# Kernel optimization log

Hardware: AMD Instinct MI355X
Metric: run time of the kernel (lower is better)

Reference implementation:

```python
import jax, jax.numpy as jnp
import numpy as np

LATENT, CTX, HID, TDIM, HEADS = 512, 512, 1024, 128, 8
HEAD_DIM = HID // HEADS
SCALE = HEAD_DIM ** -0.5


def _ln(x, g, b, eps=1e-5):
    m = jnp.mean(x, axis=-1, keepdims=True)
    v = jnp.mean((x - m) ** 2, axis=-1, keepdims=True)
    return (x - m) * jax.lax.rsqrt(v + eps) * g + b


def _time_embed(t):
    half = TDIM // 2
    exponent = jnp.linspace(0.0, 1.0, half, dtype=t.dtype)
    freqs = jnp.exp(jnp.log(1000.0) * exponent)
    ang = 2.0 * jnp.pi * t[:, None] * freqs[None, :]
    return jnp.concatenate([jnp.sin(ang), jnp.cos(ang)], axis=-1)  # [B, TDIM]


def setup_inputs() -> dict:
    key = jax.random.key(0)
    ks = iter(jax.random.split(key, 32))
    B, M = 4096, 64

    def w(k, i, o):
        return jax.random.normal(k, (i, o), jnp.float32) * 0.02

    inp = {
        "states": jax.random.normal(next(ks), (B, LATENT), jnp.float32),
        "time_values": jax.random.uniform(next(ks), (B,), jnp.float32),
        "class_summary": jax.random.normal(next(ks), (B, CTX), jnp.float32),
        "support_memory": jax.random.normal(next(ks), (B, M, LATENT), jnp.float32),
        # state_trunk: LN(latent+tdim) -> Linear -> GELU -> Linear
        "trunk_ln_g": jnp.ones((LATENT + TDIM,)), "trunk_ln_b": jnp.zeros((LATENT + TDIM,)),
        "trunk_w1": w(next(ks), LATENT + TDIM, HID), "trunk_b1": jnp.zeros((HID,)),
        "trunk_w2": w(next(ks), HID, HID), "trunk_b2": jnp.zeros((HID,)),
        # memory adapter: LN(latent) -> Linear(latent, hid)
        "mem_ln_g": jnp.ones((LATENT,)), "mem_ln_b": jnp.zeros((LATENT,)),
        "mem_w": w(next(ks), LATENT, HID), "mem_b": jnp.zeros((HID,)),
        # attention projections
        "wq": w(next(ks), HID, HID), "bq": jnp.zeros((HID,)),
        "wk": w(next(ks), HID, HID), "bk": jnp.zeros((HID,)),
        "wv": w(next(ks), HID, HID), "bv": jnp.zeros((HID,)),
        "wo": w(next(ks), HID, HID), "bo": jnp.zeros((HID,)),
        # pre-condition norm + FiLM
        "pre_ln_g": jnp.ones((HID,)), "pre_ln_b": jnp.zeros((HID,)),
        "film_w": w(next(ks), CTX, 2 * HID), "film_b": jnp.zeros((2 * HID,)),
        # conditioner: LN -> Linear -> GELU -> Linear
        "cond_ln_g": jnp.ones((HID,)), "cond_ln_b": jnp.zeros((HID,)),
        "cond_w1": w(next(ks), HID, HID), "cond_b1": jnp.zeros((HID,)),
        "cond_w2": w(next(ks), HID, HID), "cond_b2": jnp.zeros((HID,)),
        # output head: LN -> Linear -> GELU -> Linear(hid, latent)
        "head_ln_g": jnp.ones((HID,)), "head_ln_b": jnp.zeros((HID,)),
        "head_w1": w(next(ks), HID, HID), "head_b1": jnp.zeros((HID,)),
        "head_w2": w(next(ks), HID, LATENT), "head_b2": jnp.zeros((LATENT,)),
    }
    return inp


def _forward(states, time_values, class_summary, support_memory,
             trunk_ln_g, trunk_ln_b, trunk_w1, trunk_b1, trunk_w2, trunk_b2,
             mem_ln_g, mem_ln_b, mem_w, mem_b,
             wq, bq, wk, bk, wv, bv, wo, bo,
             pre_ln_g, pre_ln_b, film_w, film_b,
             cond_ln_g, cond_ln_b, cond_w1, cond_b1, cond_w2, cond_b2,
             head_ln_g, head_ln_b, head_w1, head_b1, head_w2, head_b2):
    B, M, _ = support_memory.shape
    gelu = lambda x: jax.nn.gelu(x, approximate=False)

    # trunk: g = Trunk([y, gamma(t)])
    te = _time_embed(time_values)
    x = _ln(jnp.concatenate([states, te], axis=-1), trunk_ln_g, trunk_ln_b)
    g = gelu(x @ trunk_w1 + trunk_b1) @ trunk_w2 + trunk_b2  # [B, HID]

    # encode memory + single-query multi-head attention
    mem_h = _ln(support_memory, mem_ln_g, mem_ln_b) @ mem_w + mem_b  # [B, M, HID]
    q = (g @ wq + bq).reshape(B, HEADS, HEAD_DIM)
    k = (mem_h @ wk + bk).reshape(B, M, HEADS, HEAD_DIM)
    v = (mem_h @ wv + bv).reshape(B, M, HEADS, HEAD_DIM)
    logits = jnp.einsum("bhd,bmhd->bhm", q, k) * SCALE
    attn = jax.nn.softmax(logits, axis=-1)
    summary = jnp.einsum("bhm,bmhd->bhd", attn, v).reshape(B, HID)
    attn_summary = summary @ wo + bo

    # FiLM conditioning
    combined = _ln(g + attn_summary, pre_ln_g, pre_ln_b)
    film = class_summary @ film_w + film_b
    scale, shift = film[:, :HID], film[:, HID:]
    combined = (1.0 + scale) * combined + shift
    cond_x = _ln(combined, cond_ln_g, cond_ln_b)
    conditioned = gelu(cond_x @ cond_w1 + cond_b1) @ cond_w2 + cond_b2 + combined

    # output head
    hx = _ln(conditioned, head_ln_g, head_ln_b)
    return gelu(hx @ head_w1 + head_b1) @ head_w2 + head_b2  # [B, LATENT]


def reference(states, time_values, class_summary, support_memory,
              trunk_ln_g, trunk_ln_b, trunk_w1, trunk_b1, trunk_w2, trunk_b2,
              mem_ln_g, mem_ln_b, mem_w, mem_b,
              wq, bq, wk, bk, wv, bv, wo, bo,
              pre_ln_g, pre_ln_b, film_w, film_b,
              cond_ln_g, cond_ln_b, cond_w1, cond_b1, cond_w2, cond_b2,
              head_ln_g, head_ln_b, head_w1, head_b1, head_w2, head_b2):
    return _forward(states, time_values, class_summary, support_memory,
                    trunk_ln_g, trunk_ln_b, trunk_w1, trunk_b1, trunk_w2, trunk_b2,
                    mem_ln_g, mem_ln_b, mem_w, mem_b,
                    wq, bq, wk, bk, wv, bv, wo, bo,
                    pre_ln_g, pre_ln_b, film_w, film_b,
                    cond_ln_g, cond_ln_b, cond_w1, cond_b1, cond_w2, cond_b2,
                    head_ln_g, head_ln_b, head_w1, head_b1, head_w2, head_b2)
```

## Files before the change

kernel.cpp:

```cpp
#include <hip/hip_runtime.h>
#include <cstdint>
#include <cstddef>

typedef unsigned short ushort_t;
typedef short s16x8 __attribute__((ext_vector_type(8)));
typedef float f32x4 __attribute__((ext_vector_type(4)));

__device__ __forceinline__ float bf2f(ushort_t h){
  union { unsigned int u; float f; } v; v.u = ((unsigned int)h) << 16; return v.f;
}
__device__ __forceinline__ ushort_t f2bf(float x){
  union { float f; unsigned int u; } v; v.f = x;
  unsigned int r = v.u + 0x7FFFu + ((v.u >> 16) & 1u);
  return (ushort_t)(r >> 16);
}
__device__ __forceinline__ float gelu_f(float x){
  return 0.5f * x * (1.0f + erff(x * 0.7071067811865475f));
}
__device__ __forceinline__ float wave_sum(float v){
  #pragma unroll
  for (int o = 32; o; o >>= 1) v += __shfl_xor(v, o);
  return v;
}
__device__ __forceinline__ void block_reduce2(float& s, float& q, float* red){
  s = wave_sum(s); q = wave_sum(q);
  int w = threadIdx.x >> 6, lane = threadIdx.x & 63, nw = blockDim.x >> 6;
  if (lane == 0){ red[w] = s; red[8 + w] = q; }
  __syncthreads();
  float ts = 0.f, tq = 0.f;
  for (int i = 0; i < nw; ++i){ ts += red[i]; tq += red[8 + i]; }
  __syncthreads();
  s = ts; q = tq;
}

#define SSLOT(cc, m) (((cc) & 56) | (((cc) & 7) ^ (((m) ^ ((m) >> 3)) & 7)))

struct TDesc { const float* in; ushort_t* out; int K; int N; int start; };
struct PrepArgs {
  const float* states; const float* tv; const float* lng; const float* lnb; ushort_t* xnb;
  TDesc t[11];
  int ntiles_end;
  int cast1_blocks;
  int cast_end;
  const float* memw; ushort_t* memwb;
  const float* csum; ushort_t* csb;
  const float* memb; const float* wv; const float* bvp; float* bv2;
};

__global__ __launch_bounds__(256) void prep_k(PrepArgs a){
  int bid = blockIdx.x, tid = threadIdx.x;
  __shared__ float buf[640];
  __shared__ float red[16];
  __shared__ float tbuf[32][33];
  if (bid < 4096){
    int row = bid;
    float t = a.tv[row];
    for (int i = tid; i < 640; i += 256){
      float v;
      if (i < 512) v = a.states[(size_t)row * 512 + i];
      else {
        int j = i - 512, jj = j & 63;
        float fr = expf(6.907755278982137f * ((float)jj * (1.0f / 63.0f)));
        float ang = 6.283185307179586f * t * fr;
        v = (j < 64) ? sinf(ang) : cosf(ang);
      }
      buf[i] = v;
    }
    __syncthreads();
    float s = 0.f, q = 0.f;
    for (int i = tid; i < 640; i += 256){ float v = buf[i]; s += v; q += v * v; }
    block_reduce2(s, q, red);
    float mean = s * (1.0f / 640.0f);
    float var = q * (1.0f / 640.0f) - mean * mean;
    float rstd = rsqrtf(var + 1e-5f);
    for (int i = tid; i < 640; i += 256)
      a.xnb[(size_t)row * 640 + i] = f2bf((buf[i] - mean) * rstd * a.lng[i] + a.lnb[i]);
    return;
  }
  bid -= 4096;
  if (bid < a.ntiles_end){
    int d = 0;
    #pragma unroll
    for (int i = 1; i < 11; ++i) if (bid >= a.t[i].start) d = i;
    TDesc td = a.t[d];
    int tile = bid - td.start;
    int tilesx = td.N >> 5;
    int n0 = (tile % tilesx) << 5, k0 = (tile / tilesx) << 5;
    int tx = tid & 31, ty = tid >> 5;
    #pragma unroll
    for (int j = 0; j < 32; j += 8)
      tbuf[ty + j][tx] = td.in[(size_t)(k0 + ty + j) * td.N + (n0 + tx)];
    __syncthreads();
    #pragma unroll
    for (int j = 0; j < 32; j += 8)
      td.out[(size_t)(n0 + ty + j) * td.K + (k0 + tx)] = f2bf(tbuf[tx][ty + j]);
  } else if (bid < a.cast_end){
    int ci = bid - a.ntiles_end;
    const float* src; ushort_t* dst; int i;
    if (ci < a.cast1_blocks){ src = a.memw; dst = a.memwb; i = ci * 1024 + tid * 4; }
    else { src = a.csum; dst = a.csb; i = (ci - a.cast1_blocks) * 1024 + tid * 4; }
    float4 v = *(const float4*)(src + i);
    union { ushort_t u[4]; uint2 p; } pk;
    pk.u[0] = f2bf(v.x); pk.u[1] = f2bf(v.y); pk.u[2] = f2bf(v.z); pk.u[3] = f2bf(v.w);
    *(uint2*)(dst + i) = pk.p;
  } else {
    int col = (bid - a.cast_end) * 256 + tid;
    float a0 = 0.f, a1 = 0.f, a2 = 0.f, a3 = 0.f;
    for (int j = 0; j < 1024; j += 4){
      a0 += a.memb[j + 0] * a.wv[(size_t)(j + 0) * 1024 + col];
      a1 += a.memb[j + 1] * a.wv[(size_t)(j + 1) * 1024 + col];
      a2 += a.memb[j + 2] * a.wv[(size_t)(j + 2) * 1024 + col];
      a3 += a.memb[j + 3] * a.wv[(size_t)(j + 3) * 1024 + col];
    }
    a.bv2[col] = a0 + a1 + a2 + a3 + a.bvp[col];
  }
}

__global__ __launch_bounds__(256) void ln_rows_k(const ushort_t* __restrict__ in, const float* __restrict__ g,
    const float* __restrict__ b, ushort_t* __restrict__ out, int D){
  int row = blockIdx.x, tid = threadIdx.x, i = tid * 4;
  __shared__ float red[16];
  union { uint2 p; ushort_t u[4]; } vv;
  vv.p = *(const uint2*)(in + (size_t)row * D + i);
  float v[4] = { bf2f(vv.u[0]), bf2f(vv.u[1]), bf2f(vv.u[2]), bf2f(vv.u[3]) };
  float s = v[0] + v[1] + v[2] + v[3];
  float q = v[0]*v[0] + v[1]*v[1] + v[2]*v[2] + v[3]*v[3];
  block_reduce2(s, q, red);
  float invD = 1.0f / (float)D;
  float mean = s * invD, var = q * invD - mean * mean, rstd = rsqrtf(var + 1e-5f);
  union { ushort_t u[4]; uint2 p; } pk;
  #pragma unroll
  for (int e = 0; e < 4; ++e) pk.u[e] = f2bf((v[e] - mean) * rstd * g[i + e] + b[i + e]);
  *(uint2*)(out + (size_t)row * D + i) = pk.p;
}

__global__ __launch_bounds__(256) void fuse_film_k(const ushort_t* __restrict__ combb, const ushort_t* __restrict__ filmb,
    const float* __restrict__ pg, const float* __restrict__ pb,
    const float* __restrict__ cg, const float* __restrict__ cb,
    ushort_t* __restrict__ c2b, ushort_t* __restrict__ cxb){
  int row = blockIdx.x, tid = threadIdx.x, i = tid * 4;
  __shared__ float red[16];
  union { uint2 p; ushort_t u[4]; } av;
  av.p = *(const uint2*)(combb + (size_t)row * 1024 + i);
  float x[4] = { bf2f(av.u[0]), bf2f(av.u[1]), bf2f(av.u[2]), bf2f(av.u[3]) };
  float s = x[0] + x[1] + x[2] + x[3];
  float q = x[0]*x[0] + x[1]*x[1] + x[2]*x[2] + x[3]*x[3];
  block_reduce2(s, q, red);
  float mean = s * (1.0f / 1024.0f), var = q * (1.0f / 1024.0f) - mean * mean;
  float rstd = rsqrtf(var + 1e-5f);
  float4 pgv = *(const float4*)(pg + i), pbv = *(const float4*)(pb + i);
  union { uint2 p; ushort_t u[4]; } scv, shv;
  scv.p = *(const uint2*)(filmb + (size_t)row * 2048 + i);
  shv.p = *(const uint2*)(filmb + (size_t)row * 2048 + 1024 + i);
  float c2[4];
  {
    float pgx[4] = { pgv.x, pgv.y, pgv.z, pgv.w };
    float pbx[4] = { pbv.x, pbv.y, pbv.z, pbv.w };
    #pragma unroll
    for (int e = 0; e < 4; ++e){
      float cc = (x[e] - mean) * rstd * pgx[e] + pbx[e];
      c2[e] = (1.0f + bf2f(scv.u[e])) * cc + bf2f(shv.u[e]);
    }
  }
  union { ushort_t u[4]; uint2 p; } pc;
  #pragma unroll
  for (int e = 0; e < 4; ++e) pc.u[e] = f2bf(c2[e]);
  *(uint2*)(c2b + (size_t)row * 1024 + i) = pc.p;
  float s2 = c2[0] + c2[1] + c2[2] + c2[3];
  float q2 = c2[0]*c2[0] + c2[1]*c2[1] + c2[2]*c2[2] + c2[3]*c2[3];
  block_reduce2(s2, q2, red);
  float m2 = s2 * (1.0f / 1024.0f), v2 = q2 * (1.0f / 1024.0f) - m2 * m2;
  float r2 = rsqrtf(v2 + 1e-5f);
  float4 cgv = *(const float4*)(cg + i), cbv = *(const float4*)(cb + i);
  union { ushort_t u[4]; uint2 p; } pk;
  pk.u[0] = f2bf((c2[0] - m2) * r2 * cgv.x + cbv.x);
  pk.u[1] = f2bf((c2[1] - m2) * r2 * cgv.y + cbv.y);
  pk.u[2] = f2bf((c2[2] - m2) * r2 * cgv.z + cbv.z);
  pk.u[3] = f2bf((c2[3] - m2) * r2 * cgv.w + cbv.w);
  *(uint2*)(cxb + (size_t)row * 1024 + i) = pk.p;
}

__global__ __launch_bounds__(256, 2) void suppattn_k(
    const float* __restrict__ support, const float* __restrict__ lgw, const float* __restrict__ lbw,
    const ushort_t* __restrict__ U, ushort_t* __restrict__ R)
{
  __shared__ ushort_t S[64 * 512];
  __shared__ ushort_t UG[9 * 512];
  __shared__ float WTf[8][65];
  __shared__ float SUMV[64], SUMSQ[64];
  __shared__ __align__(16) float MEANR[64];
  __shared__ __align__(16) float RSTDR[64];
  __shared__ float PMAX[4][8], PSUM[4][8], PMU[4][8];
  __shared__ float AB[2][8];
  __shared__ float MUH[8];

  int bb = blockIdx.x, tid = threadIdx.x, w = tid >> 6, l = tid & 63;
  const ushort_t* Ub = U + (size_t)bb * 4096;

  for (int id = tid; id < 576; id += 256){
    int hr8 = id >> 6, cc = id & 63;
    int byteoff = hr8 * 1024 + (((cc & 56) | ((cc & 7) ^ (hr8 & 7))) << 4);
    uint4* dst = (uint4*)((char*)UG + byteoff);
    if (hr8 < 8){
      s16x8 uv = *(const s16x8*)(Ub + hr8 * 512 + cc * 8);
      float4 g0 = *(const float4*)(lgw + cc * 8);
      float4 g1 = *(const float4*)(lgw + cc * 8 + 4);
      float ga[8] = { g0.x, g0.y, g0.z, g0.w, g1.x, g1.y, g1.z, g1.w };
      union { ushort_t u[8]; uint4 p; } pk;
      #pragma unroll
      for (int e = 0; e < 8; ++e) pk.u[e] = f2bf(ga[e] * bf2f((ushort_t)uv[e]));
      *dst = pk.p;
    } else {
      *dst = make_uint4(0x3F803F80u, 0x3F803F80u, 0x3F803F80u, 0x3F803F80u);
    }
  }

  {
    int h0 = 2 * w, h1 = 2 * w + 1;
    s16x8 u0 = *(const s16x8*)(Ub + h0 * 512 + l * 8);
    s16x8 u1 = *(const s16x8*)(Ub + h1 * 512 + l * 8);
    float4 g0 = *(const float4*)(lgw + l * 8), g1 = *(const float4*)(lgw + l * 8 + 4);
    float4 c0 = *(const float4*)(lbw + l * 8), c1 = *(const float4*)(lbw + l * 8 + 4);
    float ga[8] = { g0.x, g0.y, g0.z, g0.w, g1.x, g1.y, g1.z, g1.w };
    float ba[8] = { c0.x, c0.y, c0.z, c0.w, c1.x, c1.y, c1.z, c1.w };
    float A0 = 0.f, B0 = 0.f, A1 = 0.f, B1 = 0.f;
    #pragma unroll
    for (int e = 0; e < 8; ++e){
      float x0 = bf2f((ushort_t)u0[e]), x1 = bf2f((ushort_t)u1[e]);
      A0 += ba[e] * x0; B0 += ga[e] * x0;
      A1 += ba[e] * x1; B1 += ga[e] * x1;
    }
    A0 = wave_sum(A0); B0 = wave_sum(B0); A1 = wave_sum(A1); B1 = wave_sum(B1);
    if (l == 0){ AB[0][h0] = A0; AB[1][h0] = B0; AB[0][h1] = A1; AB[1][h1] = B1; }
  }

  #pragma unroll 4
  for (int i = 0; i < 16; ++i){
    int m = i * 4 + w;
    const float* row = support + ((size_t)bb * 64 + m) * 512 + l * 8;
    float4 a0 = *(const float4*)row, a1 = *(const float4*)(row + 4);
    union { ushort_t u[8]; uint4 p; } pk;
    pk.u[0] = f2bf(a0.x); pk.u[1] = f2bf(a0.y); pk.u[2] = f2bf(a0.z); pk.u[3] = f2bf(a0.w);
    pk.u[4] = f2bf(a1.x); pk.u[5] = f2bf(a1.y); pk.u[6] = f2bf(a1.z); pk.u[7] = f2bf(a1.w);
    int byteoff = m * 1024 + (SSLOT(l, m) << 4);
    *(uint4*)((char*)S + byteoff) = pk.p;
  }
  __syncthreads();

  int l15 = l & 15, lk = l >> 4;
  int hr = (l15 < 8) ? l15 : 8;
  int arowb = (w * 16 + l15) * 1024;
  int hrowb = hr * 1024;
  int am = w * 16 + l15;
  f32x4 dacc = (f32x4){0.f, 0.f, 0.f, 0.f};
  f32x4 sacc = (f32x4){0.f, 0.f, 0.f, 0.f};
  #pragma unroll
  for (int ks = 0; ks < 16; ++ks){
    int cc = ks * 4 + lk;
    s16x8 afr = *(const s16x8*)((char*)S + arowb + (SSLOT(cc, am) << 4));
    s16x8 bfr = *(const s16x8*)((char*)UG + hrowb + (((cc & 56) | ((cc & 7) ^ (hr & 7))) << 4));
    dacc = __builtin_amdgcn_mfma_f32_16x16x32_bf16(afr, bfr, dacc, 0, 0, 0);
    sacc = __builtin_amdgcn_mfma_f32_16x16x32_bf16(afr, afr, sacc, 0, 0, 0);
  }
  if (l15 == 8){
    #pragma unroll
    for (int j = 0; j < 4; ++j) SUMV[w * 16 + lk * 4 + j] = dacc[j];
  }
  if ((l15 >> 2) == lk) SUMSQ[w * 16 + l15] = sacc[l15 & 3];
  __syncthreads();
  if (tid < 64){
    float mean = SUMV[tid] * (1.0f / 512.0f);
    float var = SUMSQ[tid] * (1.0f / 512.0f) - mean * mean;
    MEANR[tid] = mean;
    RSTDR[tid] = rsqrtf(var + 1e-5f);
  }
  __syncthreads();

  int r0 = w * 16 + lk * 4;
  float4 mns = *(const float4*)(MEANR + r0);
  float4 rst = *(const float4*)(RSTDR + r0);
  float mn[4] = { mns.x, mns.y, mns.z, mns.w };
  float rs[4] = { rst.x, rst.y, rst.z, rst.w };
  float Ah = AB[0][l15 & 7], Bh = AB[1][l15 & 7];
  float lg[4];
  #pragma unroll
  for (int j = 0; j < 4; ++j)
    lg[j] = 0.08838834764831845f * (rs[j] * (dacc[j] - mn[j] * Bh) + Ah);
  float lmax = fmaxf(fmaxf(lg[0], lg[1]), fmaxf(lg[2], lg[3]));
  lmax = fmaxf(lmax, __shfl_xor(lmax, 16));
  lmax = fmaxf(lmax, __shfl_xor(lmax, 32));
  if (l < 8) PMAX[w][l] = lmax;
  __syncthreads();
  float gmax = fmaxf(fmaxf(PMAX[0][l15 & 7], PMAX[1][l15 & 7]),
                     fmaxf(PMAX[2][l15 & 7], PMAX[3][l15 & 7]));
  float e4[4]; float ls = 0.f, lm = 0.f;
  #pragma unroll
  for (int j = 0; j < 4; ++j){
    e4[j] = __expf(lg[j] - gmax);
    ls += e4[j];
    lm += e4[j] * rs[j] * mn[j];
  }
  ls += __shfl_xor(ls, 16); ls += __shfl_xor(ls, 32);
  lm += __shfl_xor(lm, 16); lm += __shfl_xor(lm, 32);
  if (l < 8){ PSUM[w][l] = ls; PMU[w][l] = lm; }
  __syncthreads();
  float Sh = PSUM[0][l15 & 7] + PSUM[1][l15 & 7] + PSUM[2][l15 & 7] + PSUM[3][l15 & 7];
  float inv = 1.0f / Sh;
  if (l15 < 8){
    #pragma unroll
    for (int j = 0; j < 4; ++j) WTf[l15][r0 + j] = e4[j] * rs[j] * inv;
  }
  if (w == 0 && l < 8){
    MUH[l] = (PMU[0][l] + PMU[1][l] + PMU[2][l] + PMU[3][l]) * inv;
  }
  __syncthreads();

  union { ushort_t u[8]; s16x8 v; } af0, af1;
  af0.v = (s16x8){0,0,0,0,0,0,0,0};
  af1.v = (s16x8){0,0,0,0,0,0,0,0};
  if (l15 < 8){
    #pragma unroll
    for (int e = 0; e < 8; ++e){
      af0.u[e] = f2bf(WTf[l15][lk * 8 + e]);
      af1.u[e] = f2bf(WTf[l15][32 + lk * 8 + e]);
    }
  }
  float mu[4];
  #pragma unroll
  for (int j = 0; j < 4; ++j) mu[j] = (lk < 2) ? MUH[lk * 4 + j] : 0.f;

  const char* Sp = (const char*)S;
  #pragma unroll
  for (int ns = 0; ns < 8; ++ns){
    int c = w * 128 + ns * 16 + l15;
    int cch = c >> 3, cb = (c & 7) * 2;
    int sb = cch & 56, cl = cch & 7;
    union { ushort_t u[8]; s16x8 v; } bf0, bf1;
    #pragma unroll
    for (int e = 0; e < 8; ++e){
      int m0 = lk * 8 + e;
      int m1 = m0 + 32;
      bf0.u[e] = *(const ushort_t*)(Sp + m0 * 1024 + ((sb | (cl ^ ((m0 ^ lk) & 7))) << 4) + cb);
      bf1.u[e] = *(const ushort_t*)(Sp + m1 * 1024 + ((sb | (cl ^ ((m1 ^ (4 + lk)) & 7))) << 4) + cb);
    }
    f32x4 cacc = (f32x4){0.f, 0.f, 0.f, 0.f};
    cacc = __builtin_amdgcn_mfma_f32_16x16x32_bf16(af0.v, bf0.v, cacc, 0, 0, 0);
    cacc = __builtin_amdgcn_mfma_f32_16x16x32_bf16(af1.v, bf1.v, cacc, 0, 0, 0);
    if (lk < 2){
      float gc = lgw[c], bc = lbw[c];
      #pragma unroll
      for (int j = 0; j < 4; ++j){
        int h = lk * 4 + j;
        R[(size_t)bb * 4096 + h * 512 + c] = f2bf(gc * (cacc[j] - mu[j]) + bc);
      }
    }
  }
}

#define GLL16(gsrc, ldst) \
  __builtin_amdgcn_global_load_lds((const __attribute__((address_space(1))) unsigned int*)(gsrc), \
                                   (__attribute__((address_space(3))) unsigned int*)(ldst), 16, 0, 0)

template<bool GELU, bool BIAS, bool WF32, bool WBF16, bool RESID>
__global__ __launch_bounds__(256, 3) void gemm_k(
    const ushort_t* __restrict__ A, int lda, long long aZ,
    const ushort_t* __restrict__ Bt, int ldb, long long bZ,
    const float* __restrict__ bias, long long biasZ,
    float* __restrict__ C, int ldc, long long cZ,
    ushort_t* __restrict__ Cb, int ldcb, long long cbZ,
    const ushort_t* __restrict__ R, int ldr,
    int M, int N, int K)
{
  __shared__ ushort_t smA[2][64 * 64];
  __shared__ ushort_t smB[2][128 * 64];
  int tid = threadIdx.x, lane = tid & 63, w = tid >> 6;
  int z = blockIdx.z;
  A  += (size_t)aZ * z;
  Bt += (size_t)bZ * z;
  if (BIAS)  bias += (size_t)biasZ * z;
  if (WF32)  C    += (size_t)cZ * z;
  if (WBF16) Cb   += (size_t)cbZ * z;

  int gx = gridDim.x, gy = gridDim.y;
  int nwg = gx * gy;
  int bx = blockIdx.x, by = blockIdx.y;
  if ((nwg & 7) == 0 && (gx & (gx - 1)) == 0){
    int lid = bx + gx * by;
    int cpx = nwg >> 3;
    int slid = (lid & 7) * cpx + (lid >> 3);
    int lgx = 31 - __clz(gx);
    bx = slid & (gx - 1);
    by = slid >> lgx;
  }
  int m0 = by * 64, n0 = bx * 128;
  int nk = K >> 6;

  auto stage = [&](int buf, int kt){
    int k0 = kt << 6;
    #pragma unroll
    for (int i = 0; i < 2; ++i){
      int c = ((w << 1) + i) * 64 + lane;
      int rowl = c >> 3, sp = c & 7;
      int sg = sp ^ (rowl & 7);
      GLL16(A + (size_t)(m0 + rowl) * lda + (k0 + sg * 8), &smA[buf][((w << 1) + i) * 512]);
    }
    #pragma unroll
    for (int i = 0; i < 4; ++i){
      int c = ((w << 2) + i) * 64 + lane;
      int rowl = c >> 3, sp = c & 7;
      int sg = sp ^ (rowl & 7);
      GLL16(Bt + (size_t)(n0 + rowl) * ldb + (k0 + sg * 8), &smB[buf][((w << 2) + i) * 512]);
    }
  };

  int qrow = w >> 1, qcol = w & 1;
  int l15 = lane & 15, lk = lane >> 4, l7 = lane & 7;
  int sb0 = ((0 + lk) ^ l7) << 4;
  int sb1 = ((4 + lk) ^ l7) << 4;
  int arow = (qrow * 32 + l15) * 128;
  int brow = (qcol * 64 + l15) * 128;

  f32x4 acc[2][4];
  #pragma unroll
  for (int m = 0; m < 2; ++m)
    #pragma unroll
    for (int n = 0; n < 4; ++n)
      acc[m][n] = (f32x4){0.f, 0.f, 0.f, 0.f};

  stage(0, 0);
  asm volatile("s_waitcnt vmcnt(0)" ::: "memory");
  __syncthreads();
  for (int kt = 0; kt < nk; ++kt){
    int cur = kt & 1;
    if (kt + 1 < nk) stage((kt + 1) & 1, kt + 1);
    const char* ab = (const char*)&smA[cur][0];
    const char* bbp = (const char*)&smB[cur][0];
    s16x8 af[2][2], bfv[4][2];
    #pragma unroll
    for (int m = 0; m < 2; ++m){
      af[m][0] = *(const s16x8*)(ab + arow + m * 2048 + sb0);
      af[m][1] = *(const s16x8*)(ab + arow + m * 2048 + sb1);
    }
    #pragma unroll
    for (int n = 0; n < 4; ++n){
      bfv[n][0] = *(const s16x8*)(bbp + brow + n * 2048 + sb0);
      bfv[n][1] = *(const s16x8*)(bbp + brow + n * 2048 + sb1);
    }
    #pragma unroll
    for (int kb = 0; kb < 2; ++kb)
      #pragma unroll
      for (int m = 0; m < 2; ++m)
        #pragma unroll
        for (int n = 0; n < 4; ++n)
          acc[m][n] = __builtin_amdgcn_mfma_f32_16x16x32_bf16(af[m][kb], bfv[n][kb], acc[m][n], 0, 0, 0);
    asm volatile("s_waitcnt vmcnt(0)" ::: "memory");
    __syncthreads();
  }

  #pragma unroll
  for (int n = 0; n < 4; ++n){
    int col = n0 + qcol * 64 + n * 16 + l15;
    float bvv = BIAS ? bias[col] : 0.0f;
    #pragma unroll
    for (int m = 0; m < 2; ++m){
      int rbase = m0 + qrow * 32 + m * 16 + lk * 4;
      #pragma unroll
      for (int r = 0; r < 4; ++r){
        float x = acc[m][n][r] + bvv;
        if (GELU) x = gelu_f(x);
        int row = rbase + r;
        if (RESID) x += bf2f(R[(size_t)row * ldr + col]);
        if (WF32)  C[(size_t)row * ldc + col] = x;
        if (WBF16) Cb[(size_t)row * ldcb + col] = f2bf(x);
      }
    }
  }
}

extern "C" void kernel_launch(void* const* d_in, const int* in_sizes, int n_in,
                              void* d_out, int out_size, void* d_ws, size_t ws_size,
                              hipStream_t stream)
{
  (void)in_sizes; (void)n_in; (void)out_size;
  const float* states      = (const float*)d_in[0];
  const float* time_values = (const float*)d_in[1];
  const float* class_sum   = (const float*)d_in[2];
  const float* support     = (const float*)d_in[3];
  const float* trunk_ln_g  = (const float*)d_in[4];
  const float* trunk_ln_b  = (const float*)d_in[5];
  const float* trunk_w1    = (const float*)d_in[6];
  const float* trunk_b1    = (const float*)d_in[7];
  const float* trunk_w2    = (const float*)d_in[8];
  const float* trunk_b2    = (const float*)d_in[9];
  const float* mem_ln_g    = (const float*)d_in[10];
  const float* mem_ln_b    = (const float*)d_in[11];
  const float* mem_w       = (const float*)d_in[12];
  const float* mem_b       = (const float*)d_in[13];
  const float* wq          = (const float*)d_in[14];
  const float* bq          = (const float*)d_in[15];
  const float* wk          = (const float*)d_in[16];
  const float* wv          = (const float*)d_in[18];
  const float* bvp         = (const float*)d_in[19];
  const float* wo          = (const float*)d_in[20];
  const float* bo          = (const float*)d_in[21];
  const float* pre_g       = (const float*)d_in[22];
  const float* pre_b       = (const float*)d_in[23];
  const float* film_w      = (const float*)d_in[24];
  const float* film_b      = (const float*)d_in[25];
  const float* cond_g      = (const float*)d_in[26];
  const float* cond_b      = (const float*)d_in[27];
  const float* cond_w1     = (const float*)d_in[28];
  const float* cond_b1     = (const float*)d_in[29];
  const float* cond_w2     = (const float*)d_in[30];
  const float* cond_b2     = (const float*)d_in[31];
  const float* head_g      = (const float*)d_in[32];
  const float* head_bb     = (const float*)d_in[33];
  const float* head_w1     = (const float*)d_in[34];
  const float* head_b1     = (const float*)d_in[35];
  const float* head_w2     = (const float*)d_in[36];
  const float* head_b2     = (const float*)d_in[37];
  float* out = (float*)d_out;

  char* ws = (char*)d_ws;
  size_t off = 0;
  auto alloc = [&](size_t bytes)->char*{
    char* p = ws + off;
    off += (bytes + 255) & ~(size_t)255;
    return p;
  };
  ushort_t* tw1T   = (ushort_t*)alloc((size_t)640 * 1024 * 2);
  ushort_t* tw2T   = (ushort_t*)alloc((size_t)1024 * 1024 * 2);
  ushort_t* wqT    = (ushort_t*)alloc((size_t)1024 * 1024 * 2);
  ushort_t* wkT    = (ushort_t*)alloc((size_t)1024 * 1024 * 2);
  ushort_t* wvT    = (ushort_t*)alloc((size_t)1024 * 1024 * 2);
  ushort_t* woT    = (ushort_t*)alloc((size_t)1024 * 1024 * 2);
  ushort_t* memw_b = (ushort_t*)alloc((size_t)512 * 1024 * 2);
  ushort_t* filmWT = (ushort_t*)alloc((size_t)512 * 2048 * 2);
  ushort_t* cw1T   = (ushort_t*)alloc((size_t)1024 * 1024 * 2);
  ushort_t* cw2T   = (ushort_t*)alloc((size_t)1024 * 1024 * 2);
  ushort_t* hw1T   = (ushort_t*)alloc((size_t)1024 * 1024 * 2);
  ushort_t* hw2T   = (ushort_t*)alloc((size_t)1024 * 512 * 2);
  ushort_t* K2     = (ushort_t*)alloc((size_t)512 * 1024 * 2);
  ushort_t* V2T    = (ushort_t*)alloc((size_t)1024 * 512 * 2);
  float*    bv2    = (float*)   alloc((size_t)1024 * 4);
  ushort_t* xnb    = (ushort_t*)alloc((size_t)4096 * 640 * 2);
  ushort_t* h1     = (ushort_t*)alloc((size_t)4096 * 1024 * 2);
  ushort_t* gb     = (ushort_t*)alloc((size_t)4096 * 1024 * 2);
  ushort_t* qb     = (ushort_t*)alloc((size_t)4096 * 1024 * 2);
  ushort_t* U      = (ushort_t*)alloc((size_t)4096 * 4096 * 2);
  ushort_t* Rb     = (ushort_t*)alloc((size_t)4096 * 4096 * 2);
  ushort_t* sumb   = (ushort_t*)alloc((size_t)4096 * 1024 * 2);
  ushort_t* combb  = (ushort_t*)alloc((size_t)4096 * 1024 * 2);
  ushort_t* csb    = (ushort_t*)alloc((size_t)4096 * 512 * 2);
  ushort_t* filmb  = (ushort_t*)alloc((size_t)4096 * 2048 * 2);
  ushort_t* c2b    = (ushort_t*)alloc((size_t)4096 * 1024 * 2);
  ushort_t* cxb    = (ushort_t*)alloc((size_t)4096 * 1024 * 2);
  ushort_t* c1     = (ushort_t*)alloc((size_t)4096 * 1024 * 2);
  ushort_t* cond2b = (ushort_t*)alloc((size_t)4096 * 1024 * 2);
  ushort_t* hxb    = (ushort_t*)alloc((size_t)4096 * 1024 * 2);
  ushort_t* h3     = (ushort_t*)alloc((size_t)4096 * 1024 * 2);
  if (off > ws_size) return;

  PrepArgs pa;
  pa.states = states; pa.tv = time_values; pa.lng = trunk_ln_g; pa.lnb = trunk_ln_b; pa.xnb = xnb;
  int s = 0;
  auto setT = [&](int i, const float* in, ushort_t* o, int K, int N){
    pa.t[i].in = in; pa.t[i].out = o; pa.t[i].K = K; pa.t[i].N = N; pa.t[i].start = s;
    s += (N >> 5) * (K >> 5);
  };
  setT(0, trunk_w1, tw1T, 640, 1024);
  setT(1, trunk_w2, tw2T, 1024, 1024);
  setT(2, wq, wqT, 1024, 1024);
  setT(3, wk, wkT, 1024, 1024);
  setT(4, wv, wvT, 1024, 1024);
  setT(5, wo, woT, 1024, 1024);
  setT(6, film_w, filmWT, 512, 2048);
  setT(7, cond_w1, cw1T, 1024, 1024);
  setT(8, cond_w2, cw2T, 1024, 1024);
  setT(9, head_w1, hw1T, 1024, 1024);
  setT(10, head_w2, hw2T, 1024, 512);
  pa.ntiles_end = s;
  pa.cast1_blocks = (512 * 1024) / 1024;
  pa.cast_end = s + pa.cast1_blocks + (4096 * 512) / 1024;
  pa.memw = mem_w; pa.memwb = memw_b;
  pa.csum = class_sum; pa.csb = csb;
  pa.memb = mem_b; pa.wv = wv; pa.bvp = bvp; pa.bv2 = bv2;
  prep_k<<<4096 + pa.cast_end + 4, 256, 0, stream>>>(pa);

  gemm_k<false, false, false, true, false><<<dim3(8, 8, 1), 256, 0, stream>>>(
      memw_b, 1024, 0, wkT, 1024, 0, nullptr, 0, nullptr, 0, 0, K2, 1024, 0, nullptr, 0, 512, 1024, 1024);
  gemm_k<false, false, false, true, false><<<dim3(4, 16, 1), 256, 0, stream>>>(
      wvT, 1024, 0, memw_b, 1024, 0, nullptr, 0, nullptr, 0, 0, V2T, 512, 0, nullptr, 0, 1024, 512, 1024);

  gemm_k<true, true, false, true, false><<<dim3(8, 64, 1), 256, 0, stream>>>(
      xnb, 640, 0, tw1T, 640, 0, trunk_b1, 0, nullptr, 0, 0, h1, 1024, 0, nullptr, 0, 4096, 1024, 640);
  gemm_k<false, true, false, true, false><<<dim3(8, 64, 1), 256, 0, stream>>>(
      h1, 1024, 0, tw2T, 1024, 0, trunk_b2, 0, nullptr, 0, 0, gb, 1024, 0, nullptr, 0, 4096, 1024, 1024);
  gemm_k<false, true, false, true, false><<<dim3(8, 64, 1), 256, 0, stream>>>(
      gb, 1024, 0, wqT, 1024, 0, bq, 0, nullptr, 0, 0, qb, 1024, 0, nullptr, 0, 4096, 1024, 1024);
  gemm_k<false, false, false, true, false><<<dim3(4, 64, 8), 256, 0, stream>>>(
      qb, 1024, 128, K2, 1024, 128, nullptr, 0, nullptr, 0, 0, U, 4096, 512, nullptr, 0, 4096, 512, 128);

  suppattn_k<<<4096, 256, 0, stream>>>(support, mem_ln_g, mem_ln_b, U, Rb);

  gemm_k<false, true, false, true, false><<<dim3(1, 64, 8), 256, 0, stream>>>(
      Rb, 4096, 512, V2T, 512, 65536, bv2, 128, nullptr, 0, 0, sumb, 1024, 128, nullptr, 0, 4096, 128, 512);

  gemm_k<false, true, false, true, true><<<dim3(8, 64, 1), 256, 0, stream>>>(
      sumb, 1024, 0, woT, 1024, 0, bo, 0, nullptr, 0, 0, combb, 1024, 0, gb, 1024, 4096, 1024, 1024);
  gemm_k<false, true, false, true, false><<<dim3(16, 64, 1), 256, 0, stream>>>(
      csb, 512, 0, filmWT, 512, 0, film_b, 0, nullptr, 0, 0, filmb, 2048, 0, nullptr, 0, 4096, 2048, 512);

  fuse_film_k<<<4096, 256, 0, stream>>>(combb, filmb, pre_g, pre_b, cond_g, cond_b, c2b, cxb);

  gemm_k<true, true, false, true, false><<<dim3(8, 64, 1), 256, 0, stream>>>(
      cxb, 1024, 0, cw1T, 1024, 0, cond_b1, 0, nullptr, 0, 0, c1, 1024, 0, nullptr, 0, 4096, 1024, 1024);
  gemm_k<false, true, false, true, true><<<dim3(8, 64, 1), 256, 0, stream>>>(
      c1, 1024, 0, cw2T, 1024, 0, cond_b2, 0, nullptr, 0, 0, cond2b, 1024, 0, c2b, 1024, 4096, 1024, 1024);
  ln_rows_k<<<4096, 256, 0, stream>>>(cond2b, head_g, head_bb, hxb, 1024);
  gemm_k<true, true, false, true, false><<<dim3(8, 64, 1), 256, 0, stream>>>(
      hxb, 1024, 0, hw1T, 1024, 0, head_b1, 0, nullptr, 0, 0, h3, 1024, 0, nullptr, 0, 4096, 1024, 1024);
  gemm_k<false, true, true, false, false><<<dim3(4, 64, 1), 256, 0, stream>>>(
      h3, 1024, 0, hw2T, 1024, 0, head_b2, 0, out, 512, 0, nullptr, 0, 0, nullptr, 0, 4096, 512, 1024);
}
```

Measured before the change: 451.8 us.

## Merge GEMM chains into persistent kernels with software grid barriers

```diff
diff --git a/kernel.cpp b/kernel.cpp
--- a/kernel.cpp
+++ b/kernel.cpp
@@ -116,70 +116,6 @@
   }
 }
 
-__global__ __launch_bounds__(256) void ln_rows_k(const ushort_t* __restrict__ in, const float* __restrict__ g,
-    const float* __restrict__ b, ushort_t* __restrict__ out, int D){
-  int row = blockIdx.x, tid = threadIdx.x, i = tid * 4;
-  __shared__ float red[16];
-  union { uint2 p; ushort_t u[4]; } vv;
-  vv.p = *(const uint2*)(in + (size_t)row * D + i);
-  float v[4] = { bf2f(vv.u[0]), bf2f(vv.u[1]), bf2f(vv.u[2]), bf2f(vv.u[3]) };
-  float s = v[0] + v[1] + v[2] + v[3];
-  float q = v[0]*v[0] + v[1]*v[1] + v[2]*v[2] + v[3]*v[3];
-  block_reduce2(s, q, red);
-  float invD = 1.0f / (float)D;
-  float mean = s * invD, var = q * invD - mean * mean, rstd = rsqrtf(var + 1e-5f);
-  union { ushort_t u[4]; uint2 p; } pk;
-  #pragma unroll
-  for (int e = 0; e < 4; ++e) pk.u[e] = f2bf((v[e] - mean) * rstd * g[i + e] + b[i + e]);
-  *(uint2*)(out + (size_t)row * D + i) = pk.p;
-}
-
-__global__ __launch_bounds__(256) void fuse_film_k(const ushort_t* __restrict__ combb, const ushort_t* __restrict__ filmb,
-    const float* __restrict__ pg, const float* __restrict__ pb,
-    const float* __restrict__ cg, const float* __restrict__ cb,
-    ushort_t* __restrict__ c2b, ushort_t* __restrict__ cxb){
-  int row = blockIdx.x, tid = threadIdx.x, i = tid * 4;
-  __shared__ float red[16];
-  union { uint2 p; ushort_t u[4]; } av;
-  av.p = *(const uint2*)(combb + (size_t)row * 1024 + i);
-  float x[4] = { bf2f(av.u[0]), bf2f(av.u[1]), bf2f(av.u[2]), bf2f(av.u[3]) };
-  float s = x[0] + x[1] + x[2] + x[3];
-  float q = x[0]*x[0] + x[1]*x[1] + x[2]*x[2] + x[3]*x[3];
-  block_reduce2(s, q, red);
-  float mean = s * (1.0f / 1024.0f), var = q * (1.0f / 1024.0f) - mean * mean;
-  float rstd = rsqrtf(var + 1e-5f);
-  float4 pgv = *(const float4*)(pg + i), pbv = *(const float4*)(pb + i);
-  union { uint2 p; ushort_t u[4]; } scv, shv;
-  scv.p = *(const uint2*)(filmb + (size_t)row * 2048 + i);
-  shv.p = *(const uint2*)(filmb + (size_t)row * 2048 + 1024 + i);
-  float c2[4];
-  {
-    float pgx[4] = { pgv.x, pgv.y, pgv.z, pgv.w };
-    float pbx[4] = { pbv.x, pbv.y, pbv.z, pbv.w };
-    #pragma unroll
-    for (int e = 0; e < 4; ++e){
-      float cc = (x[e] - mean) * rstd * pgx[e] + pbx[e];
-      c2[e] = (1.0f + bf2f(scv.u[e])) * cc + bf2f(shv.u[e]);
-    }
-  }
-  union { ushort_t u[4]; uint2 p; } pc;
-  #pragma unroll
-  for (int e = 0; e < 4; ++e) pc.u[e] = f2bf(c2[e]);
-  *(uint2*)(c2b + (size_t)row * 1024 + i) = pc.p;
-  float s2 = c2[0] + c2[1] + c2[2] + c2[3];
-  float q2 = c2[0]*c2[0] + c2[1]*c2[1] + c2[2]*c2[2] + c2[3]*c2[3];
-  block_reduce2(s2, q2, red);
-  float m2 = s2 * (1.0f / 1024.0f), v2 = q2 * (1.0f / 1024.0f) - m2 * m2;
-  float r2 = rsqrtf(v2 + 1e-5f);
-  float4 cgv = *(const float4*)(cg + i), cbv = *(const float4*)(cb + i);
-  union { ushort_t u[4]; uint2 p; } pk;
-  pk.u[0] = f2bf((c2[0] - m2) * r2 * cgv.x + cbv.x);
-  pk.u[1] = f2bf((c2[1] - m2) * r2 * cgv.y + cbv.y);
-  pk.u[2] = f2bf((c2[2] - m2) * r2 * cgv.z + cbv.z);
-  pk.u[3] = f2bf((c2[3] - m2) * r2 * cgv.w + cbv.w);
-  *(uint2*)(cxb + (size_t)row * 1024 + i) = pk.p;
-}
-
 __global__ __launch_bounds__(256, 2) void suppattn_k(
     const float* __restrict__ support, const float* __restrict__ lgw, const float* __restrict__ lbw,
     const ushort_t* __restrict__ U, ushort_t* __restrict__ R)
@@ -196,6 +132,18 @@
 
   int bb = blockIdx.x, tid = threadIdx.x, w = tid >> 6, l = tid & 63;
   const ushort_t* Ub = U + (size_t)bb * 4096;
+
+  #pragma unroll 4
+  for (int i = 0; i < 16; ++i){
+    int m = i * 4 + w;
+    const float* row = support + ((size_t)bb * 64 + m) * 512 + l * 8;
+    float4 a0 = *(const float4*)row, a1 = *(const float4*)(row + 4);
+    union { ushort_t u[8]; uint4 p; } pk;
+    pk.u[0] = f2bf(a0.x); pk.u[1] = f2bf(a0.y); pk.u[2] = f2bf(a0.z); pk.u[3] = f2bf(a0.w);
+    pk.u[4] = f2bf(a1.x); pk.u[5] = f2bf(a1.y); pk.u[6] = f2bf(a1.z); pk.u[7] = f2bf(a1.w);
+    int byteoff = m * 1024 + (SSLOT(l, m) << 4);
+    *(uint4*)((char*)S + byteoff) = pk.p;
+  }
 
   for (int id = tid; id < 576; id += 256){
     int hr8 = id >> 6, cc = id & 63;
@@ -233,18 +181,6 @@
     A0 = wave_sum(A0); B0 = wave_sum(B0); A1 = wave_sum(A1); B1 = wave_sum(B1);
     if (l == 0){ AB[0][h0] = A0; AB[1][h0] = B0; AB[0][h1] = A1; AB[1][h1] = B1; }
   }
-
-  #pragma unroll 4
-  for (int i = 0; i < 16; ++i){
-    int m = i * 4 + w;
-    const float* row = support + ((size_t)bb * 64 + m) * 512 + l * 8;
-    float4 a0 = *(const float4*)row, a1 = *(const float4*)(row + 4);
-    union { ushort_t u[8]; uint4 p; } pk;
-    pk.u[0] = f2bf(a0.x); pk.u[1] = f2bf(a0.y); pk.u[2] = f2bf(a0.z); pk.u[3] = f2bf(a0.w);
-    pk.u[4] = f2bf(a1.x); pk.u[5] = f2bf(a1.y); pk.u[6] = f2bf(a1.z); pk.u[7] = f2bf(a1.w);
-    int byteoff = m * 1024 + (SSLOT(l, m) << 4);
-    *(uint4*)((char*)S + byteoff) = pk.p;
-  }
   __syncthreads();
 
   int l15 = l & 15, lk = l >> 4;
@@ -361,39 +297,58 @@
   __builtin_amdgcn_global_load_lds((const __attribute__((address_space(1))) unsigned int*)(gsrc), \
                                    (__attribute__((address_space(3))) unsigned int*)(ldst), 16, 0, 0)
 
-template<bool GELU, bool BIAS, bool WF32, bool WBF16, bool RESID>
-__global__ __launch_bounds__(256, 3) void gemm_k(
-    const ushort_t* __restrict__ A, int lda, long long aZ,
-    const ushort_t* __restrict__ Bt, int ldb, long long bZ,
-    const float* __restrict__ bias, long long biasZ,
-    float* __restrict__ C, int ldc, long long cZ,
-    ushort_t* __restrict__ Cb, int ldcb, long long cbZ,
-    const ushort_t* __restrict__ R, int ldr,
-    int M, int N, int K)
-{
-  __shared__ ushort_t smA[2][64 * 64];
-  __shared__ ushort_t smB[2][128 * 64];
+struct Seg {
+  const ushort_t* A; const ushort_t* Bt; const float* bias;
+  ushort_t* Cb; float* Cf; const ushort_t* R;
+  int lda, ldb, ldc, ldr, gx, K, flags, startTile;
+};
+#define MAXSEG 14
+#define MAXSTG 8
+struct CoopArgs {
+  Seg seg[MAXSEG];
+  int stage_seg_start[MAXSTG + 1];
+  int stage_ntiles[MAXSTG];
+  int stage_type[MAXSTG];
+  int nstages;
+  unsigned* bar;
+  const ushort_t* combb; const ushort_t* filmb;
+  const float *pg, *pb, *cg, *cbp;
+  ushort_t *c2b, *cxb;
+  const ushort_t* ln_in; const float *ln_g, *ln_b; ushort_t* ln_out;
+};
+
+__device__ __forceinline__ void gbar(unsigned* bar, int nb){
+  __syncthreads();
+  if (threadIdx.x == 0){
+    __threadfence();
+    int x = blockIdx.x & 7;
+    int q = nb >> 3;
+    unsigned gen = __hip_atomic_load(&bar[144], __ATOMIC_ACQUIRE, __HIP_MEMORY_SCOPE_AGENT);
+    unsigned v = __hip_atomic_fetch_add(&bar[x * 16], 1u, __ATOMIC_ACQ_REL, __HIP_MEMORY_SCOPE_AGENT);
+    if ((int)v == q - 1){
+      __hip_atomic_store(&bar[x * 16], 0u, __ATOMIC_RELAXED, __HIP_MEMORY_SCOPE_AGENT);
+      unsigned d = __hip_atomic_fetch_add(&bar[128], 1u, __ATOMIC_ACQ_REL, __HIP_MEMORY_SCOPE_AGENT);
+      if (d == 7u){
+        __hip_atomic_store(&bar[128], 0u, __ATOMIC_RELAXED, __HIP_MEMORY_SCOPE_AGENT);
+        __hip_atomic_fetch_add(&bar[144], 1u, __ATOMIC_RELEASE, __HIP_MEMORY_SCOPE_AGENT);
+      } else {
+        while (__hip_atomic_load(&bar[144], __ATOMIC_ACQUIRE, __HIP_MEMORY_SCOPE_AGENT) == gen)
+          __builtin_amdgcn_s_sleep(2);
+      }
+    } else {
+      while (__hip_atomic_load(&bar[144], __ATOMIC_ACQUIRE, __HIP_MEMORY_SCOPE_AGENT) == gen)
+        __builtin_amdgcn_s_sleep(2);
+    }
+    __threadfence();
+  }
+  __syncthreads();
+}
+
+__device__ __forceinline__ void gemm_tile(ushort_t (*smA)[4096], ushort_t (*smB)[4096],
+                                          const Seg& g, int m0, int n0){
+  __syncthreads();
   int tid = threadIdx.x, lane = tid & 63, w = tid >> 6;
-  int z = blockIdx.z;
-  A  += (size_t)aZ * z;
-  Bt += (size_t)bZ * z;
-  if (BIAS)  bias += (size_t)biasZ * z;
-  if (WF32)  C    += (size_t)cZ * z;
-  if (WBF16) Cb   += (size_t)cbZ * z;
-
-  int gx = gridDim.x, gy = gridDim.y;
-  int nwg = gx * gy;
-  int bx = blockIdx.x, by = blockIdx.y;
-  if ((nwg & 7) == 0 && (gx & (gx - 1)) == 0){
-    int lid = bx + gx * by;
-    int cpx = nwg >> 3;
-    int slid = (lid & 7) * cpx + (lid >> 3);
-    int lgx = 31 - __clz(gx);
-    bx = slid & (gx - 1);
-    by = slid >> lgx;
-  }
-  int m0 = by * 64, n0 = bx * 128;
-  int nk = K >> 6;
+  int nk = g.K >> 6;
 
   auto stage = [&](int buf, int kt){
     int k0 = kt << 6;
@@ -402,14 +357,14 @@
       int c = ((w << 1) + i) * 64 + lane;
       int rowl = c >> 3, sp = c & 7;
       int sg = sp ^ (rowl & 7);
-      GLL16(A + (size_t)(m0 + rowl) * lda + (k0 + sg * 8), &smA[buf][((w << 1) + i) * 512]);
-    }
-    #pragma unroll
-    for (int i = 0; i < 4; ++i){
-      int c = ((w << 2) + i) * 64 + lane;
+      GLL16(g.A + (size_t)(m0 + rowl) * g.lda + (k0 + sg * 8), &smA[buf][((w << 1) + i) * 512]);
+    }
+    #pragma unroll
+    for (int i = 0; i < 2; ++i){
+      int c = ((w << 1) + i) * 64 + lane;
       int rowl = c >> 3, sp = c & 7;
       int sg = sp ^ (rowl & 7);
-      GLL16(Bt + (size_t)(n0 + rowl) * ldb + (k0 + sg * 8), &smB[buf][((w << 2) + i) * 512]);
+      GLL16(g.Bt + (size_t)(n0 + rowl) * g.ldb + (k0 + sg * 8), &smB[buf][((w << 1) + i) * 512]);
     }
   };
 
@@ -418,13 +373,13 @@
   int sb0 = ((0 + lk) ^ l7) << 4;
   int sb1 = ((4 + lk) ^ l7) << 4;
   int arow = (qrow * 32 + l15) * 128;
-  int brow = (qcol * 64 + l15) * 128;
-
-  f32x4 acc[2][4];
+  int brow = (qcol * 32 + l15) * 128;
+
+  f32x4 acc[2][2];
   #pragma unroll
   for (int m = 0; m < 2; ++m)
     #pragma unroll
-    for (int n = 0; n < 4; ++n)
+    for (int n = 0; n < 2; ++n)
       acc[m][n] = (f32x4){0.f, 0.f, 0.f, 0.f};
 
   stage(0, 0);
@@ -435,14 +390,14 @@
     if (kt + 1 < nk) stage((kt + 1) & 1, kt + 1);
     const char* ab = (const char*)&smA[cur][0];
     const char* bbp = (const char*)&smB[cur][0];
-    s16x8 af[2][2], bfv[4][2];
+    s16x8 af[2][2], bfv[2][2];
     #pragma unroll
     for (int m = 0; m < 2; ++m){
       af[m][0] = *(const s16x8*)(ab + arow + m * 2048 + sb0);
       af[m][1] = *(const s16x8*)(ab + arow + m * 2048 + sb1);
     }
     #pragma unroll
-    for (int n = 0; n < 4; ++n){
+    for (int n = 0; n < 2; ++n){
       bfv[n][0] = *(const s16x8*)(bbp + brow + n * 2048 + sb0);
       bfv[n][1] = *(const s16x8*)(bbp + brow + n * 2048 + sb1);
     }
@@ -451,29 +406,120 @@
       #pragma unroll
       for (int m = 0; m < 2; ++m)
         #pragma unroll
-        for (int n = 0; n < 4; ++n)
+        for (int n = 0; n < 2; ++n)
           acc[m][n] = __builtin_amdgcn_mfma_f32_16x16x32_bf16(af[m][kb], bfv[n][kb], acc[m][n], 0, 0, 0);
-    asm volatile("s_waitcnt vmcnt(0)" ::: "memory");
-    __syncthreads();
-  }
-
-  #pragma unroll
-  for (int n = 0; n < 4; ++n){
-    int col = n0 + qcol * 64 + n * 16 + l15;
-    float bvv = BIAS ? bias[col] : 0.0f;
+    if (kt + 1 < nk){
+      asm volatile("s_waitcnt vmcnt(0)" ::: "memory");
+      __syncthreads();
+    }
+  }
+
+  bool fG = g.flags & 1, fB = g.flags & 2, fF = g.flags & 4, fR = g.flags & 16;
+  #pragma unroll
+  for (int n = 0; n < 2; ++n){
+    int col = n0 + qcol * 32 + n * 16 + l15;
+    float bvv = fB ? g.bias[col] : 0.0f;
     #pragma unroll
     for (int m = 0; m < 2; ++m){
       int rbase = m0 + qrow * 32 + m * 16 + lk * 4;
       #pragma unroll
       for (int r = 0; r < 4; ++r){
         float x = acc[m][n][r] + bvv;
-        if (GELU) x = gelu_f(x);
+        if (fG) x = gelu_f(x);
         int row = rbase + r;
-        if (RESID) x += bf2f(R[(size_t)row * ldr + col]);
-        if (WF32)  C[(size_t)row * ldc + col] = x;
-        if (WBF16) Cb[(size_t)row * ldcb + col] = f2bf(x);
+        if (fR) x += bf2f(g.R[(size_t)row * g.ldr + col]);
+        if (fF) g.Cf[(size_t)row * g.ldc + col] = x;
+        else    g.Cb[(size_t)row * g.ldc + col] = f2bf(x);
       }
     }
+  }
+}
+
+__device__ void film_row(const CoopArgs& a, int row, float* red){
+  int tid = threadIdx.x, i = tid * 4;
+  union { uint2 p; ushort_t u[4]; } av;
+  av.p = *(const uint2*)(a.combb + (size_t)row * 1024 + i);
+  float x[4] = { bf2f(av.u[0]), bf2f(av.u[1]), bf2f(av.u[2]), bf2f(av.u[3]) };
+  float s = x[0] + x[1] + x[2] + x[3];
+  float q = x[0]*x[0] + x[1]*x[1] + x[2]*x[2] + x[3]*x[3];
+  block_reduce2(s, q, red);
+  float mean = s * (1.0f / 1024.0f), var = q * (1.0f / 1024.0f) - mean * mean;
+  float rstd = rsqrtf(var + 1e-5f);
+  float4 pgv = *(const float4*)(a.pg + i), pbv = *(const float4*)(a.pb + i);
+  union { uint2 p; ushort_t u[4]; } scv, shv;
+  scv.p = *(const uint2*)(a.filmb + (size_t)row * 2048 + i);
+  shv.p = *(const uint2*)(a.filmb + (size_t)row * 2048 + 1024 + i);
+  float c2[4];
+  {
+    float pgx[4] = { pgv.x, pgv.y, pgv.z, pgv.w };
+    float pbx[4] = { pbv.x, pbv.y, pbv.z, pbv.w };
+    #pragma unroll
+    for (int e = 0; e < 4; ++e){
+      float cc = (x[e] - mean) * rstd * pgx[e] + pbx[e];
+      c2[e] = (1.0f + bf2f(scv.u[e])) * cc + bf2f(shv.u[e]);
+    }
+  }
+  union { ushort_t u[4]; uint2 p; } pc;
+  #pragma unroll
+  for (int e = 0; e < 4; ++e) pc.u[e] = f2bf(c2[e]);
+  *(uint2*)(a.c2b + (size_t)row * 1024 + i) = pc.p;
+  float s2 = c2[0] + c2[1] + c2[2] + c2[3];
+  float q2 = c2[0]*c2[0] + c2[1]*c2[1] + c2[2]*c2[2] + c2[3]*c2[3];
+  block_reduce2(s2, q2, red);
+  float m2 = s2 * (1.0f / 1024.0f), v2 = q2 * (1.0f / 1024.0f) - m2 * m2;
+  float r2 = rsqrtf(v2 + 1e-5f);
+  float4 cgv = *(const float4*)(a.cg + i), cbv = *(const float4*)(a.cbp + i);
+  union { ushort_t u[4]; uint2 p; } pk;
+  pk.u[0] = f2bf((c2[0] - m2) * r2 * cgv.x + cbv.x);
+  pk.u[1] = f2bf((c2[1] - m2) * r2 * cgv.y + cbv.y);
+  pk.u[2] = f2bf((c2[2] - m2) * r2 * cgv.z + cbv.z);
+  pk.u[3] = f2bf((c2[3] - m2) * r2 * cgv.w + cbv.w);
+  *(uint2*)(a.cxb + (size_t)row * 1024 + i) = pk.p;
+}
+
+__device__ void ln_row(const CoopArgs& a, int row, float* red){
+  int tid = threadIdx.x, i = tid * 4;
+  union { uint2 p; ushort_t u[4]; } vv;
+  vv.p = *(const uint2*)(a.ln_in + (size_t)row * 1024 + i);
+  float v[4] = { bf2f(vv.u[0]), bf2f(vv.u[1]), bf2f(vv.u[2]), bf2f(vv.u[3]) };
+  float s = v[0] + v[1] + v[2] + v[3];
+  float q = v[0]*v[0] + v[1]*v[1] + v[2]*v[2] + v[3]*v[3];
+  block_reduce2(s, q, red);
+  float mean = s * (1.0f / 1024.0f), var = q * (1.0f / 1024.0f) - mean * mean;
+  float rstd = rsqrtf(var + 1e-5f);
+  union { ushort_t u[4]; uint2 p; } pk;
+  #pragma unroll
+  for (int e = 0; e < 4; ++e) pk.u[e] = f2bf((v[e] - mean) * rstd * a.ln_g[i + e] + a.ln_b[i + e]);
+  *(uint2*)(a.ln_out + (size_t)row * 1024 + i) = pk.p;
+}
+
+__global__ __launch_bounds__(256, 4) void coop_k(CoopArgs a){
+  __shared__ ushort_t smA[2][4096];
+  __shared__ ushort_t smB[2][4096];
+  __shared__ float red[16];
+  int nb = gridDim.x, bid = blockIdx.x;
+  int q = nb >> 3;
+  int slid = (bid & 7) * q + (bid >> 3);
+
+  for (int st = 0; st < a.nstages; ++st){
+    int type = a.stage_type[st];
+    if (type == 0){
+      int s0 = a.stage_seg_start[st], s1 = a.stage_seg_start[st + 1];
+      int nt = a.stage_ntiles[st];
+      for (int t = slid; t < nt; t += nb){
+        int si = s0;
+        while (si + 1 < s1 && t >= a.seg[si + 1].startTile) ++si;
+        Seg g = a.seg[si];
+        int tl = t - g.startTile;
+        int bx = tl % g.gx, by = tl / g.gx;
+        gemm_tile(smA, smB, g, by * 64, bx * 64);
+      }
+    } else if (type == 1){
+      for (int row = bid; row < 4096; row += nb) film_row(a, row, red);
+    } else {
+      for (int row = bid; row < 4096; row += nb) ln_row(a, row, red);
+    }
+    if (st + 1 < a.nstages) gbar(a.bar, nb);
   }
 }
 
@@ -559,7 +605,10 @@
   ushort_t* cond2b = (ushort_t*)alloc((size_t)4096 * 1024 * 2);
   ushort_t* hxb    = (ushort_t*)alloc((size_t)4096 * 1024 * 2);
   ushort_t* h3     = (ushort_t*)alloc((size_t)4096 * 1024 * 2);
+  unsigned* bar    = (unsigned*)alloc(1024);
   if (off > ws_size) return;
+
+  hipMemsetAsync(bar, 0, 1024, stream);
 
   PrepArgs pa;
   pa.states = states; pa.tv = time_values; pa.lng = trunk_ln_g; pa.lnb = trunk_ln_b; pa.xnb = xnb;
@@ -587,39 +636,65 @@
   pa.memb = mem_b; pa.wv = wv; pa.bvp = bvp; pa.bv2 = bv2;
   prep_k<<<4096 + pa.cast_end + 4, 256, 0, stream>>>(pa);
 
-  gemm_k<false, false, false, true, false><<<dim3(8, 8, 1), 256, 0, stream>>>(
-      memw_b, 1024, 0, wkT, 1024, 0, nullptr, 0, nullptr, 0, 0, K2, 1024, 0, nullptr, 0, 512, 1024, 1024);
-  gemm_k<false, false, false, true, false><<<dim3(4, 16, 1), 256, 0, stream>>>(
-      wvT, 1024, 0, memw_b, 1024, 0, nullptr, 0, nullptr, 0, 0, V2T, 512, 0, nullptr, 0, 1024, 512, 1024);
-
-  gemm_k<true, true, false, true, false><<<dim3(8, 64, 1), 256, 0, stream>>>(
-      xnb, 640, 0, tw1T, 640, 0, trunk_b1, 0, nullptr, 0, 0, h1, 1024, 0, nullptr, 0, 4096, 1024, 640);
-  gemm_k<false, true, false, true, false><<<dim3(8, 64, 1), 256, 0, stream>>>(
-      h1, 1024, 0, tw2T, 1024, 0, trunk_b2, 0, nullptr, 0, 0, gb, 1024, 0, nullptr, 0, 4096, 1024, 1024);
-  gemm_k<false, true, false, true, false><<<dim3(8, 64, 1), 256, 0, stream>>>(
-      gb, 1024, 0, wqT, 1024, 0, bq, 0, nullptr, 0, 0, qb, 1024, 0, nullptr, 0, 4096, 1024, 1024);
-  gemm_k<false, false, false, true, false><<<dim3(4, 64, 8), 256, 0, stream>>>(
-      qb, 1024, 128, K2, 1024, 128, nullptr, 0, nullptr, 0, 0, U, 4096, 512, nullptr, 0, 4096, 512, 128);
+  int occ = 0;
+  int nb = 256;
+  if (hipOccupancyMaxActiveBlocksPerMultiprocessor(&occ, coop_k, 256, 0) == hipSuccess && occ >= 1){
+    nb = occ * 256;
+    if (nb > 1024) nb = 1024;
+  }
+  nb &= ~7;
+  if (nb < 8) nb = 8;
+
+  auto mkseg = [](const ushort_t* A, const ushort_t* Bt, const float* bias, ushort_t* Cb, float* Cf,
+                  const ushort_t* R, int lda, int ldb, int ldc, int ldr, int gx, int K, int flags, int start)->Seg{
+    Seg g; g.A = A; g.Bt = Bt; g.bias = bias; g.Cb = Cb; g.Cf = Cf; g.R = R;
+    g.lda = lda; g.ldb = ldb; g.ldc = ldc; g.ldr = ldr; g.gx = gx; g.K = K; g.flags = flags; g.startTile = start;
+    return g;
+  };
+
+  {
+    CoopArgs a{};
+    a.seg[0]  = mkseg(memw_b, wkT, nullptr, K2, nullptr, nullptr, 1024, 1024, 1024, 0, 16, 1024, 0, 0);
+    a.seg[1]  = mkseg(wvT, memw_b, nullptr, V2T, nullptr, nullptr, 1024, 1024, 512, 0, 8, 1024, 0, 128);
+    a.seg[2]  = mkseg(csb, filmWT, film_b, filmb, nullptr, nullptr, 512, 512, 2048, 0, 32, 512, 2, 256);
+    a.seg[3]  = mkseg(xnb, tw1T, trunk_b1, h1, nullptr, nullptr, 640, 640, 1024, 0, 16, 640, 1|2, 2304);
+    a.seg[4]  = mkseg(h1, tw2T, trunk_b2, gb, nullptr, nullptr, 1024, 1024, 1024, 0, 16, 1024, 2, 0);
+    a.seg[5]  = mkseg(gb, wqT, bq, qb, nullptr, nullptr, 1024, 1024, 1024, 0, 16, 1024, 2, 0);
+    for (int z = 0; z < 8; ++z)
+      a.seg[6 + z] = mkseg(qb + z * 128, K2 + z * 128, nullptr, U + z * 512, nullptr, nullptr,
+                           1024, 1024, 4096, 0, 8, 128, 0, z * 512);
+    int sss[5] = {0, 4, 5, 6, 14};
+    int snt[4] = {3328, 1024, 1024, 4096};
+    for (int i = 0; i < 5; ++i) a.stage_seg_start[i] = sss[i];
+    for (int i = 0; i < 4; ++i){ a.stage_ntiles[i] = snt[i]; a.stage_type[i] = 0; }
+    a.nstages = 4;
+    a.bar = bar;
+    coop_k<<<nb, 256, 0, stream>>>(a);
+  }
 
   suppattn_k<<<4096, 256, 0, stream>>>(support, mem_ln_g, mem_ln_b, U, Rb);
 
-  gemm_k<false, true, false, true, false><<<dim3(1, 64, 8), 256, 0, stream>>>(
-      Rb, 4096, 512, V2T, 512, 65536, bv2, 128, nullptr, 0, 0, sumb, 1024, 128, nullptr, 0, 4096, 128, 512);
-
-  gemm_k<false, true, false, true, true><<<dim3(8, 64, 1), 256, 0, stream>>>(
-      sumb, 1024, 0, woT, 1024, 0, bo, 0, nullptr, 0, 0, combb, 1024, 0, gb, 1024, 4096, 1024, 1024);
-  gemm_k<false, true, false, true, false><<<dim3(16, 64, 1), 256, 0, stream>>>(
-      csb, 512, 0, filmWT, 512, 0, film_b, 0, nullptr, 0, 0, filmb, 2048, 0, nullptr, 0, 4096, 2048, 512);
-
-  fuse_film_k<<<4096, 256, 0, stream>>>(combb, filmb, pre_g, pre_b, cond_g, cond_b, c2b, cxb);
-
-  gemm_k<true, true, false, true, false><<<dim3(8, 64, 1), 256, 0, stream>>>(
-      cxb, 1024, 0, cw1T, 1024, 0, cond_b1, 0, nullptr, 0, 0, c1, 1024, 0, nullptr, 0, 4096, 1024, 1024);
-  gemm_k<false, true, false, true, true><<<dim3(8, 64, 1), 256, 0, stream>>>(
-      c1, 1024, 0, cw2T, 1024, 0, cond_b2, 0, nullptr, 0, 0, cond2b, 1024, 0, c2b, 1024, 4096, 1024, 1024);
-  ln_rows_k<<<4096, 256, 0, stream>>>(cond2b, head_g, head_bb, hxb, 1024);
-  gemm_k<true, true, false, true, false><<<dim3(8, 64, 1), 256, 0, stream>>>(
-      hxb, 1024, 0, hw1T, 1024, 0, head_b1, 0, nullptr, 0, 0, h3, 1024, 0, nullptr, 0, 4096, 1024, 1024);
-  gemm_k<false, true, true, false, false><<<dim3(4, 64, 1), 256, 0, stream>>>(
-      h3, 1024, 0, hw2T, 1024, 0, head_b2, 0, out, 512, 0, nullptr, 0, 0, nullptr, 0, 4096, 512, 1024);
-}
+  {
+    CoopArgs a{};
+    for (int z = 0; z < 8; ++z)
+      a.seg[z] = mkseg(Rb + z * 512, V2T + (size_t)z * 65536, bv2 + z * 128, sumb + z * 128, nullptr, nullptr,
+                       4096, 512, 1024, 0, 2, 512, 2, z * 128);
+    a.seg[8]  = mkseg(sumb, woT, bo, combb, nullptr, gb, 1024, 1024, 1024, 1024, 16, 1024, 2|16, 0);
+    a.seg[9]  = mkseg(cxb, cw1T, cond_b1, c1, nullptr, nullptr, 1024, 1024, 1024, 0, 16, 1024, 1|2, 0);
+    a.seg[10] = mkseg(c1, cw2T, cond_b2, cond2b, nullptr, c2b, 1024, 1024, 1024, 1024, 16, 1024, 2|16, 0);
+    a.seg[11] = mkseg(hxb, hw1T, head_b1, h3, nullptr, nullptr, 1024, 1024, 1024, 0, 16, 1024, 1|2, 0);
+    a.seg[12] = mkseg(h3, hw2T, head_b2, nullptr, out, nullptr, 1024, 1024, 512, 0, 8, 1024, 2|4, 0);
+    int sss[9] = {0, 8, 9, 9, 10, 11, 11, 12, 13};
+    int snt[8] = {1024, 1024, 0, 1024, 1024, 0, 1024, 512};
+    int sty[8] = {0, 0, 1, 0, 0, 2, 0, 0};
+    for (int i = 0; i < 9; ++i) a.stage_seg_start[i] = sss[i];
+    for (int i = 0; i < 8; ++i){ a.stage_ntiles[i] = snt[i]; a.stage_type[i] = sty[i]; }
+    a.nstages = 8;
+    a.bar = bar;
+    a.combb = combb; a.filmb = filmb;
+    a.pg = pre_g; a.pb = pre_b; a.cg = cond_g; a.cbp = cond_b;
+    a.c2b = c2b; a.cxb = cxb;
+    a.ln_in = cond2b; a.ln_g = head_g; a.ln_b = head_bb; a.ln_out = hxb;
+    coop_k<<<nb, 256, 0, stream>>>(a);
+  }
+}
```

Result: slower. 1.073 ms (+137.4%).
